# Performance work log

Hardware: AMD Instinct MI355X
Metric: run time of the kernel (lower is better)

The kernel has to match this reference:

```python
import jax, jax.numpy as jnp
import numpy as np

VOCAB = 1024
HIDDEN = 512
EMBED = 256
EPS = 1e-12  # F.normalize default eps


def setup_inputs() -> dict:
    key = jax.random.key(0)
    ks = jax.random.split(key, 7)
    B, T = 64, 16384
    tokens = jax.random.randint(ks[0], (B, T), 0, VOCAB, dtype=jnp.int64)
    # Linear params (torch nn.Linear: y = x @ W.T + b); store as [in, out] for einsum
    def lin(k, fan_in, fan_out):
        bound = 1.0 / np.sqrt(fan_in)
        kw, kb = jax.random.split(k)
        W = jax.random.uniform(kw, (fan_in, fan_out), minval=-bound, maxval=bound, dtype=jnp.float32)
        b = jax.random.uniform(kb, (fan_out,), minval=-bound, maxval=bound, dtype=jnp.float32)
        return W, b
    W1, b1 = lin(ks[1], VOCAB, HIDDEN)
    W2, b2 = lin(ks[2], HIDDEN, HIDDEN)
    W3, b3 = lin(ks[3], HIDDEN, EMBED)
    return {"tokens": tokens, "W1": W1, "b1": b1, "W2": W2, "b2": b2, "W3": W3, "b3": b3}


def reference(tokens, W1, b1, W2, b2, W3, b3):
    B, T = tokens.shape
    idx = jnp.mod(tokens, VOCAB)  # tokens % 1024
    # one_hot(...).mean(dim=1) == per-row token histogram / T; computed via scatter-add
    counts = jnp.zeros((B, VOCAB), jnp.float32).at[
        jnp.arange(B)[:, None], idx
    ].add(1.0)
    pooled = counts / jnp.asarray(T, jnp.float32)  # [B, 1024]
    h = jax.nn.relu(pooled @ W1 + b1)
    h = jax.nn.relu(h @ W2 + b2)
    emb = h @ W3 + b3  # [B, 256]
    norm = jnp.linalg.norm(emb, axis=-1, keepdims=True)
    return emb / jnp.maximum(norm, EPS)
```

## Files before the change

### kernel.cpp

```cpp
#include <hip/hip_runtime.h>
#include <hip/hip_bf16.h>


#define VOCAB 1024
#define HIDDEN 512
#define EMBED 256
#define TOK_T 16384
#define BATCH 64
#define HSEG 4

#define AGENT __HIP_MEMORY_SCOPE_AGENT

struct alignas(128) Flag { unsigned v; };

__device__ __forceinline__ void st_u32(unsigned* p, unsigned v) {
    __hip_atomic_store(p, v, __ATOMIC_RELAXED, AGENT);
}
__device__ __forceinline__ void st_f32(float* p, float v) {
    __hip_atomic_store(p, v, __ATOMIC_RELAXED, AGENT);
}

__device__ __forceinline__ void signal(Flag* flag) {
    asm volatile("s_waitcnt vmcnt(0)" ::: "memory");
    __syncthreads();
    if (threadIdx.x == 0) __hip_atomic_fetch_add(&flag->v, 1u, __ATOMIC_RELAXED, AGENT);
}
__device__ __forceinline__ void wait_flag(const Flag* flag, unsigned target) {
    if (threadIdx.x == 0) {
        while (__hip_atomic_load(&flag->v, __ATOMIC_RELAXED, AGENT) != target)
            __builtin_amdgcn_s_sleep(1);
    }
    __syncthreads();
}

#define XSIDX(k) ((k) + ((k) >> 6))

struct SMemDense {
    float4 xs4[VOCAB + VOCAB / 64];
    float part[16][4][32];
};
union SMem {
    unsigned cnt[VOCAB];
    SMemDense d;
};

template <int K, int OUT, bool RELU, bool SSQ>
__device__ __forceinline__ void dense_phase(SMem& sm, int rg, int jw,
                                            const float* __restrict__ in,
                                            const float* __restrict__ W,
                                            const float* __restrict__ bias,
                                            float* __restrict__ outp,
                                            float* __restrict__ ssqp) {
    constexpr int KG = 16;
    constexpr int KC = K / KG;
    constexpr int JW = OUT / 32;
    const int b0 = rg * 4;
    const int tid = threadIdx.x;

    for (int k = tid; k < K; k += 256) {
        float4 v;
        v.x = in[(size_t)(b0 + 0) * K + k];
        v.y = in[(size_t)(b0 + 1) * K + k];
        v.z = in[(size_t)(b0 + 2) * K + k];
        v.w = in[(size_t)(b0 + 3) * K + k];
        sm.d.xs4[XSIDX(k)] = v;
    }
    __syncthreads();

    const int jt = tid & 15;
    const int kg = tid >> 4;
    const float* __restrict__ w = W + (size_t)(kg * KC) * OUT + jw * 32 + jt * 2;

    float2 acc0 = {0.f, 0.f}, acc1 = {0.f, 0.f}, acc2 = {0.f, 0.f}, acc3 = {0.f, 0.f};
#pragma unroll 8
    for (int ks = 0; ks < KC; ++ks) {
        const int k = kg * KC + ks;
        const float4 xv = sm.d.xs4[XSIDX(k)];
        const float2 wv = *(const float2*)(w + (size_t)ks * OUT);
        acc0.x = fmaf(xv.x, wv.x, acc0.x); acc0.y = fmaf(xv.x, wv.y, acc0.y);
        acc1.x = fmaf(xv.y, wv.x, acc1.x); acc1.y = fmaf(xv.y, wv.y, acc1.y);
        acc2.x = fmaf(xv.z, wv.x, acc2.x); acc2.y = fmaf(xv.z, wv.y, acc2.y);
        acc3.x = fmaf(xv.w, wv.x, acc3.x); acc3.y = fmaf(xv.w, wv.y, acc3.y);
    }

    *(float2*)&sm.d.part[kg][0][jt * 2] = acc0;
    *(float2*)&sm.d.part[kg][1][jt * 2] = acc1;
    *(float2*)&sm.d.part[kg][2][jt * 2] = acc2;
    *(float2*)&sm.d.part[kg][3][jt * 2] = acc3;
    __syncthreads();

    if (tid < 128) {
        const int r = tid >> 5;
        const int jl = tid & 31;
        float s = bias[jw * 32 + jl];
#pragma unroll
        for (int g = 0; g < KG; ++g) s += sm.d.part[g][r][jl];
        if (RELU) s = fmaxf(s, 0.0f);
        st_f32(&outp[(size_t)(b0 + r) * OUT + jw * 32 + jl], s);
        if constexpr (SSQ) {
            float s2 = s * s;
#pragma unroll
            for (int off = 16; off > 0; off >>= 1) s2 += __shfl_down(s2, off, 32);
            if (jl == 0) st_f32(&ssqp[(size_t)(b0 + r) * JW + jw], s2);
        }
    }
}

__global__ __launch_bounds__(256) void fused_kernel(const int* __restrict__ tokens,
                                                    const float* __restrict__ W1,
                                                    const float* __restrict__ b1,
                                                    const float* __restrict__ W2,
                                                    const float* __restrict__ b2,
                                                    const float* __restrict__ W3,
                                                    const float* __restrict__ b3,
                                                    float* __restrict__ out,
                                                    unsigned* __restrict__ counts,
                                                    float* __restrict__ h1,
                                                    float* __restrict__ h2,
                                                    float* __restrict__ emb,
                                                    float* __restrict__ ssqp,
                                                    Flag* __restrict__ flagH,
                                                    Flag* __restrict__ flag1,
                                                    Flag* __restrict__ flag2,
                                                    Flag* __restrict__ flag3) {
    __shared__ SMem sm;
    const int blk = blockIdx.x;
    const int tid = threadIdx.x;

    {
        const int b = blk >> 2;
        const int seg = blk & 3;
#pragma unroll
        for (int i = 0; i < VOCAB / 256; ++i) sm.cnt[tid + 256 * i] = 0u;
        __syncthreads();

        const int4* __restrict__ t4 =
            reinterpret_cast<const int4*>(tokens + (size_t)b * TOK_T + seg * (TOK_T / HSEG));
#pragma unroll
        for (int i = 0; i < TOK_T / HSEG / 4 / 256; ++i) {
            int4 v = t4[i * 256 + tid];
            atomicAdd(&sm.cnt[v.x & (VOCAB - 1)], 1u);
            atomicAdd(&sm.cnt[v.y & (VOCAB - 1)], 1u);
            atomicAdd(&sm.cnt[v.z & (VOCAB - 1)], 1u);
            atomicAdd(&sm.cnt[v.w & (VOCAB - 1)], 1u);
        }
        __syncthreads();

        unsigned* __restrict__ row = counts + ((size_t)b * HSEG + seg) * VOCAB;
#pragma unroll
        for (int i = 0; i < 4; ++i) st_u32(&row[tid * 4 + i], sm.cnt[tid * 4 + i]);
        signal(&flagH[b]);
    }

    {
        const int rg = blk >> 4;
        const int jw = blk & 15;
        const int b0 = rg * 4;
        if (tid == 0) {
#pragma unroll
            for (int r = 0; r < 4; ++r)
                while (__hip_atomic_load(&flagH[b0 + r].v, __ATOMIC_RELAXED, AGENT) != HSEG)
                    __builtin_amdgcn_s_sleep(1);
        }
        __syncthreads();

        {
            const float invT = 1.0f / (float)TOK_T;
#pragma unroll
            for (int ko = 0; ko < 4; ++ko) {
                const int k = tid + 256 * ko;
                float4 v;
#pragma unroll
                for (int r = 0; r < 4; ++r) {
                    const unsigned* __restrict__ cr = counts + (size_t)(b0 + r) * HSEG * VOCAB;
                    unsigned s = cr[k] + cr[k + VOCAB] + cr[k + 2 * VOCAB] + cr[k + 3 * VOCAB];
                    (&v.x)[r] = (float)s * invT;
                }
                sm.d.xs4[XSIDX(k)] = v;
            }
        }
        __syncthreads();

        constexpr int K = VOCAB, OUT = HIDDEN, KG = 16, KC = K / KG;
        const int jt = tid & 15;
        const int kg = tid >> 4;
        const float* __restrict__ w = W1 + (size_t)(kg * KC) * OUT + jw * 32 + jt * 2;
        float2 acc0 = {0.f, 0.f}, acc1 = {0.f, 0.f}, acc2 = {0.f, 0.f}, acc3 = {0.f, 0.f};
#pragma unroll 8
        for (int ks = 0; ks < KC; ++ks) {
            const int k = kg * KC + ks;
            const float4 xv = sm.d.xs4[XSIDX(k)];
            const float2 wv = *(const float2*)(w + (size_t)ks * OUT);
            acc0.x = fmaf(xv.x, wv.x, acc0.x); acc0.y = fmaf(xv.x, wv.y, acc0.y);
            acc1.x = fmaf(xv.y, wv.x, acc1.x); acc1.y = fmaf(xv.y, wv.y, acc1.y);
            acc2.x = fmaf(xv.z, wv.x, acc2.x); acc2.y = fmaf(xv.z, wv.y, acc2.y);
            acc3.x = fmaf(xv.w, wv.x, acc3.x); acc3.y = fmaf(xv.w, wv.y, acc3.y);
        }
        *(float2*)&sm.d.part[kg][0][jt * 2] = acc0;
        *(float2*)&sm.d.part[kg][1][jt * 2] = acc1;
        *(float2*)&sm.d.part[kg][2][jt * 2] = acc2;
        *(float2*)&sm.d.part[kg][3][jt * 2] = acc3;
        __syncthreads();
        if (tid < 128) {
            const int r = tid >> 5;
            const int jl = tid & 31;
            float s = b1[jw * 32 + jl];
#pragma unroll
            for (int g = 0; g < KG; ++g) s += sm.d.part[g][r][jl];
            st_f32(&h1[(size_t)(b0 + r) * OUT + jw * 32 + jl], fmaxf(s, 0.0f));
        }
        signal(&flag1[rg]);
    }

    {
        const int rg = blk >> 4;
        const int jw = blk & 15;
        wait_flag(&flag1[rg], 16);
        dense_phase<HIDDEN, HIDDEN, true, false>(sm, rg, jw, h1, W2, b2, h2, nullptr);
        signal(&flag2[rg]);
    }

    if (blk < (BATCH / 4) * (EMBED / 32)) {
        const int rg = blk >> 3;
        const int jw = blk & 7;
        wait_flag(&flag2[rg], 16);
        dense_phase<HIDDEN, EMBED, false, true>(sm, rg, jw, h2, W3, b3, emb, ssqp);
        signal(&flag3[rg]);
    }

    if (blk < BATCH) {
        const int b = blk;
        wait_flag(&flag3[b >> 2], 8);
        float total = 0.0f;
#pragma unroll
        for (int i = 0; i < EMBED / 32; ++i) total += ssqp[(size_t)b * (EMBED / 32) + i];
        const float v = emb[(size_t)b * EMBED + tid];
        out[(size_t)b * EMBED + tid] = v / fmaxf(sqrtf(total), 1e-12f);
    }
}

extern "C" void kernel_launch(void* const* d_in, const int* in_sizes, int n_in,
                              void* d_out, int out_size, void* d_ws, size_t ws_size,
                              hipStream_t stream) {
    const int*   tokens = (const int*)d_in[0];
    const float* W1     = (const float*)d_in[1];
    const float* b1     = (const float*)d_in[2];
    const float* W2     = (const float*)d_in[3];
    const float* b2     = (const float*)d_in[4];
    const float* W3     = (const float*)d_in[5];
    const float* b3     = (const float*)d_in[6];
    float*       out    = (float*)d_out;

    uint8_t* base = (uint8_t*)d_ws;
    unsigned* counts = (unsigned*)(base);
    float*    h1     = (float*)(base + 0x100000);
    float*    h2     = (float*)(base + 0x120000);
    float*    emb    = (float*)(base + 0x140000);
    float*    ssqp   = (float*)(base + 0x150000);
    Flag*     flagH  = (Flag*)(base + 0x150800);
    Flag*     flag1  = flagH + BATCH;
    Flag*     flag2  = flag1 + 16;
    Flag*     flag3  = flag2 + 16;

    hipMemsetAsync((void*)flagH, 0, 112 * sizeof(Flag), stream);

    fused_kernel<<<256, 256, 0, stream>>>(tokens, W1, b1, W2, b2, W3, b3, out,
                                          counts, h1, h2, emb, ssqp,
                                          flagH, flag1, flag2, flag3);
}
```

Before: 28.40 us.

## Double block count to 512 with 2-row groups and fused final normalization

Doubles the grid from 256 to 512 blocks: histograms split each row into 8 segments, and the dense layers handle 2 batch rows per block instead of 4. This spreads weight streaming and token counting across more CUs. The separate normalization phase is folded into the last finishing block of each layer-3 row group, detected with a fetch-add ticket, which removes one flag wait stage. Smaller row groups mean each W column tile is re-read from memory by twice as many blocks, and the grid-wide spin waits now assume all 512 blocks are resident at once.

```diff
diff --git a/kernel.cpp b/kernel.cpp
--- a/kernel.cpp
+++ b/kernel.cpp
@@ -7,7 +7,7 @@
 #define EMBED 256
 #define TOK_T 16384
 #define BATCH 64
-#define HSEG 4
+#define HSEG 8
 
 #define AGENT __HIP_MEMORY_SCOPE_AGENT
 
@@ -25,19 +25,16 @@
     __syncthreads();
     if (threadIdx.x == 0) __hip_atomic_fetch_add(&flag->v, 1u, __ATOMIC_RELAXED, AGENT);
 }
-__device__ __forceinline__ void wait_flag(const Flag* flag, unsigned target) {
-    if (threadIdx.x == 0) {
-        while (__hip_atomic_load(&flag->v, __ATOMIC_RELAXED, AGENT) != target)
-            __builtin_amdgcn_s_sleep(1);
-    }
-    __syncthreads();
-}
-
-#define XSIDX(k) ((k) + ((k) >> 6))
+__device__ __forceinline__ void spin(const Flag* flag, unsigned target) {
+    while (__hip_atomic_load(&flag->v, __ATOMIC_RELAXED, AGENT) != target)
+        __builtin_amdgcn_s_sleep(1);
+}
+
+#define XSIDX(k) ((k) + ((k) >> 5))
 
 struct SMemDense {
-    float4 xs4[VOCAB + VOCAB / 64];
-    float part[16][4][32];
+    float2 xs2[VOCAB + VOCAB / 32];
+    float part[16][2][32];
 };
 union SMem {
     unsigned cnt[VOCAB];
@@ -45,51 +42,33 @@
 };
 
 template <int K, int OUT, bool RELU, bool SSQ>
-__device__ __forceinline__ void dense_phase(SMem& sm, int rg, int jw,
-                                            const float* __restrict__ in,
-                                            const float* __restrict__ W,
-                                            const float* __restrict__ bias,
-                                            float* __restrict__ outp,
-                                            float* __restrict__ ssqp) {
+__device__ __forceinline__ void dense_core(SMem& sm, int rg, int jw,
+                                           const float* __restrict__ W,
+                                           const float* __restrict__ bias,
+                                           float* __restrict__ outp,
+                                           float* __restrict__ ssqp) {
     constexpr int KG = 16;
     constexpr int KC = K / KG;
-    constexpr int JW = OUT / 32;
-    const int b0 = rg * 4;
+    const int b0 = rg * 2;
     const int tid = threadIdx.x;
-
-    for (int k = tid; k < K; k += 256) {
-        float4 v;
-        v.x = in[(size_t)(b0 + 0) * K + k];
-        v.y = in[(size_t)(b0 + 1) * K + k];
-        v.z = in[(size_t)(b0 + 2) * K + k];
-        v.w = in[(size_t)(b0 + 3) * K + k];
-        sm.d.xs4[XSIDX(k)] = v;
-    }
-    __syncthreads();
-
     const int jt = tid & 15;
     const int kg = tid >> 4;
     const float* __restrict__ w = W + (size_t)(kg * KC) * OUT + jw * 32 + jt * 2;
 
-    float2 acc0 = {0.f, 0.f}, acc1 = {0.f, 0.f}, acc2 = {0.f, 0.f}, acc3 = {0.f, 0.f};
+    float2 a0 = {0.f, 0.f}, a1 = {0.f, 0.f};
 #pragma unroll 8
     for (int ks = 0; ks < KC; ++ks) {
         const int k = kg * KC + ks;
-        const float4 xv = sm.d.xs4[XSIDX(k)];
+        const float2 x = sm.d.xs2[XSIDX(k)];
         const float2 wv = *(const float2*)(w + (size_t)ks * OUT);
-        acc0.x = fmaf(xv.x, wv.x, acc0.x); acc0.y = fmaf(xv.x, wv.y, acc0.y);
-        acc1.x = fmaf(xv.y, wv.x, acc1.x); acc1.y = fmaf(xv.y, wv.y, acc1.y);
-        acc2.x = fmaf(xv.z, wv.x, acc2.x); acc2.y = fmaf(xv.z, wv.y, acc2.y);
-        acc3.x = fmaf(xv.w, wv.x, acc3.x); acc3.y = fmaf(xv.w, wv.y, acc3.y);
-    }
-
-    *(float2*)&sm.d.part[kg][0][jt * 2] = acc0;
-    *(float2*)&sm.d.part[kg][1][jt * 2] = acc1;
-    *(float2*)&sm.d.part[kg][2][jt * 2] = acc2;
-    *(float2*)&sm.d.part[kg][3][jt * 2] = acc3;
+        a0.x = fmaf(x.x, wv.x, a0.x); a0.y = fmaf(x.x, wv.y, a0.y);
+        a1.x = fmaf(x.y, wv.x, a1.x); a1.y = fmaf(x.y, wv.y, a1.y);
+    }
+    *(float2*)&sm.d.part[kg][0][jt * 2] = a0;
+    *(float2*)&sm.d.part[kg][1][jt * 2] = a1;
     __syncthreads();
 
-    if (tid < 128) {
+    if (tid < 64) {
         const int r = tid >> 5;
         const int jl = tid & 31;
         float s = bias[jw * 32 + jl];
@@ -101,7 +80,7 @@
             float s2 = s * s;
 #pragma unroll
             for (int off = 16; off > 0; off >>= 1) s2 += __shfl_down(s2, off, 32);
-            if (jl == 0) st_f32(&ssqp[(size_t)(b0 + r) * JW + jw], s2);
+            if (jl == 0) st_f32(&ssqp[(size_t)(b0 + r) * 8 + jw], s2);
         }
     }
 }
@@ -124,12 +103,13 @@
                                                     Flag* __restrict__ flag2,
                                                     Flag* __restrict__ flag3) {
     __shared__ SMem sm;
+    __shared__ unsigned lastf;
     const int blk = blockIdx.x;
     const int tid = threadIdx.x;
 
     {
-        const int b = blk >> 2;
-        const int seg = blk & 3;
+        const int b = blk >> 3;
+        const int seg = blk & 7;
 #pragma unroll
         for (int i = 0; i < VOCAB / 256; ++i) sm.cnt[tid + 256 * i] = 0u;
         __syncthreads();
@@ -138,7 +118,7 @@
             reinterpret_cast<const int4*>(tokens + (size_t)b * TOK_T + seg * (TOK_T / HSEG));
 #pragma unroll
         for (int i = 0; i < TOK_T / HSEG / 4 / 256; ++i) {
-            int4 v = t4[i * 256 + tid];
+            int4 v = t4[tid + 256 * i];
             atomicAdd(&sm.cnt[v.x & (VOCAB - 1)], 1u);
             atomicAdd(&sm.cnt[v.y & (VOCAB - 1)], 1u);
             atomicAdd(&sm.cnt[v.z & (VOCAB - 1)], 1u);
@@ -148,19 +128,18 @@
 
         unsigned* __restrict__ row = counts + ((size_t)b * HSEG + seg) * VOCAB;
 #pragma unroll
-        for (int i = 0; i < 4; ++i) st_u32(&row[tid * 4 + i], sm.cnt[tid * 4 + i]);
+        for (int i = 0; i < VOCAB / 256; ++i)
+            st_u32(&row[tid + 256 * i], sm.cnt[tid + 256 * i]);
         signal(&flagH[b]);
     }
 
     {
         const int rg = blk >> 4;
         const int jw = blk & 15;
-        const int b0 = rg * 4;
+        const int b0 = rg * 2;
         if (tid == 0) {
-#pragma unroll
-            for (int r = 0; r < 4; ++r)
-                while (__hip_atomic_load(&flagH[b0 + r].v, __ATOMIC_RELAXED, AGENT) != HSEG)
-                    __builtin_amdgcn_s_sleep(1);
+            spin(&flagH[b0], HSEG);
+            spin(&flagH[b0 + 1], HSEG);
         }
         __syncthreads();
 
@@ -169,73 +148,80 @@
 #pragma unroll
             for (int ko = 0; ko < 4; ++ko) {
                 const int k = tid + 256 * ko;
-                float4 v;
-#pragma unroll
-                for (int r = 0; r < 4; ++r) {
-                    const unsigned* __restrict__ cr = counts + (size_t)(b0 + r) * HSEG * VOCAB;
-                    unsigned s = cr[k] + cr[k + VOCAB] + cr[k + 2 * VOCAB] + cr[k + 3 * VOCAB];
-                    (&v.x)[r] = (float)s * invT;
+                unsigned s0 = 0, s1 = 0;
+#pragma unroll
+                for (int sg = 0; sg < HSEG; ++sg) {
+                    s0 += counts[((size_t)(b0 + 0) * HSEG + sg) * VOCAB + k];
+                    s1 += counts[((size_t)(b0 + 1) * HSEG + sg) * VOCAB + k];
                 }
-                sm.d.xs4[XSIDX(k)] = v;
+                float2 v = {(float)s0 * invT, (float)s1 * invT};
+                sm.d.xs2[XSIDX(k)] = v;
             }
         }
         __syncthreads();
 
-        constexpr int K = VOCAB, OUT = HIDDEN, KG = 16, KC = K / KG;
-        const int jt = tid & 15;
-        const int kg = tid >> 4;
-        const float* __restrict__ w = W1 + (size_t)(kg * KC) * OUT + jw * 32 + jt * 2;
-        float2 acc0 = {0.f, 0.f}, acc1 = {0.f, 0.f}, acc2 = {0.f, 0.f}, acc3 = {0.f, 0.f};
-#pragma unroll 8
-        for (int ks = 0; ks < KC; ++ks) {
-            const int k = kg * KC + ks;
-            const float4 xv = sm.d.xs4[XSIDX(k)];
-            const float2 wv = *(const float2*)(w + (size_t)ks * OUT);
-            acc0.x = fmaf(xv.x, wv.x, acc0.x); acc0.y = fmaf(xv.x, wv.y, acc0.y);
-            acc1.x = fmaf(xv.y, wv.x, acc1.x); acc1.y = fmaf(xv.y, wv.y, acc1.y);
-            acc2.x = fmaf(xv.z, wv.x, acc2.x); acc2.y = fmaf(xv.z, wv.y, acc2.y);
-            acc3.x = fmaf(xv.w, wv.x, acc3.x); acc3.y = fmaf(xv.w, wv.y, acc3.y);
-        }
-        *(float2*)&sm.d.part[kg][0][jt * 2] = acc0;
-        *(float2*)&sm.d.part[kg][1][jt * 2] = acc1;
-        *(float2*)&sm.d.part[kg][2][jt * 2] = acc2;
-        *(float2*)&sm.d.part[kg][3][jt * 2] = acc3;
-        __syncthreads();
-        if (tid < 128) {
-            const int r = tid >> 5;
-            const int jl = tid & 31;
-            float s = b1[jw * 32 + jl];
-#pragma unroll
-            for (int g = 0; g < KG; ++g) s += sm.d.part[g][r][jl];
-            st_f32(&h1[(size_t)(b0 + r) * OUT + jw * 32 + jl], fmaxf(s, 0.0f));
-        }
+        dense_core<VOCAB, HIDDEN, true, false>(sm, rg, jw, W1, b1, h1, nullptr);
         signal(&flag1[rg]);
     }
 
     {
         const int rg = blk >> 4;
         const int jw = blk & 15;
-        wait_flag(&flag1[rg], 16);
-        dense_phase<HIDDEN, HIDDEN, true, false>(sm, rg, jw, h1, W2, b2, h2, nullptr);
+        const int b0 = rg * 2;
+        if (tid == 0) spin(&flag1[rg], 16);
+        __syncthreads();
+
+#pragma unroll
+        for (int ko = 0; ko < 2; ++ko) {
+            const int k = tid + 256 * ko;
+            float2 v;
+            v.x = h1[(size_t)(b0 + 0) * HIDDEN + k];
+            v.y = h1[(size_t)(b0 + 1) * HIDDEN + k];
+            sm.d.xs2[XSIDX(k)] = v;
+        }
+        __syncthreads();
+
+        dense_core<HIDDEN, HIDDEN, true, false>(sm, rg, jw, W2, b2, h2, nullptr);
         signal(&flag2[rg]);
     }
 
-    if (blk < (BATCH / 4) * (EMBED / 32)) {
+    if (blk < 256) {
         const int rg = blk >> 3;
         const int jw = blk & 7;
-        wait_flag(&flag2[rg], 16);
-        dense_phase<HIDDEN, EMBED, false, true>(sm, rg, jw, h2, W3, b3, emb, ssqp);
-        signal(&flag3[rg]);
-    }
-
-    if (blk < BATCH) {
-        const int b = blk;
-        wait_flag(&flag3[b >> 2], 8);
-        float total = 0.0f;
-#pragma unroll
-        for (int i = 0; i < EMBED / 32; ++i) total += ssqp[(size_t)b * (EMBED / 32) + i];
-        const float v = emb[(size_t)b * EMBED + tid];
-        out[(size_t)b * EMBED + tid] = v / fmaxf(sqrtf(total), 1e-12f);
+        const int b0 = rg * 2;
+        if (tid == 0) spin(&flag2[rg], 16);
+        __syncthreads();
+
+#pragma unroll
+        for (int ko = 0; ko < 2; ++ko) {
+            const int k = tid + 256 * ko;
+            float2 v;
+            v.x = h2[(size_t)(b0 + 0) * HIDDEN + k];
+            v.y = h2[(size_t)(b0 + 1) * HIDDEN + k];
+            sm.d.xs2[XSIDX(k)] = v;
+        }
+        __syncthreads();
+
+        dense_core<HIDDEN, EMBED, false, true>(sm, rg, jw, W3, b3, emb, ssqp);
+
+        asm volatile("s_waitcnt vmcnt(0)" ::: "memory");
+        __syncthreads();
+        if (tid == 0)
+            lastf = (__hip_atomic_fetch_add(&flag3[rg].v, 1u, __ATOMIC_RELAXED, AGENT) == 7u);
+        __syncthreads();
+
+        if (lastf) {
+            const int r = tid >> 7;
+            const int j2 = (tid & 127) * 2;
+            float total = 0.0f;
+#pragma unroll
+            for (int i = 0; i < 8; ++i) total += ssqp[(size_t)(b0 + r) * 8 + i];
+            const float scale = 1.0f / fmaxf(sqrtf(total), 1e-12f);
+            const float e0 = emb[(size_t)(b0 + r) * EMBED + j2];
+            const float e1 = emb[(size_t)(b0 + r) * EMBED + j2 + 1];
+            out[(size_t)(b0 + r) * EMBED + j2] = e0 * scale;
+            out[(size_t)(b0 + r) * EMBED + j2 + 1] = e1 * scale;
+        }
     }
 }
 
@@ -253,18 +239,18 @@
 
     uint8_t* base = (uint8_t*)d_ws;
     unsigned* counts = (unsigned*)(base);
-    float*    h1     = (float*)(base + 0x100000);
-    float*    h2     = (float*)(base + 0x120000);
-    float*    emb    = (float*)(base + 0x140000);
-    float*    ssqp   = (float*)(base + 0x150000);
-    Flag*     flagH  = (Flag*)(base + 0x150800);
+    float*    h1     = (float*)(base + 0x200000);
+    float*    h2     = (float*)(base + 0x220000);
+    float*    emb    = (float*)(base + 0x240000);
+    float*    ssqp   = (float*)(base + 0x250000);
+    Flag*     flagH  = (Flag*)(base + 0x250800);
     Flag*     flag1  = flagH + BATCH;
-    Flag*     flag2  = flag1 + 16;
-    Flag*     flag3  = flag2 + 16;
-
-    hipMemsetAsync((void*)flagH, 0, 112 * sizeof(Flag), stream);
-
-    fused_kernel<<<256, 256, 0, stream>>>(tokens, W1, b1, W2, b2, W3, b3, out,
+    Flag*     flag2  = flag1 + 32;
+    Flag*     flag3  = flag2 + 32;
+
+    hipMemsetAsync((void*)flagH, 0, 160 * sizeof(Flag), stream);
+
+    fused_kernel<<<512, 256, 0, stream>>>(tokens, W1, b1, W2, b2, W3, b3, out,
                                           counts, h1, h2, emb, ssqp,
                                           flagH, flag1, flag2, flag3);
 }
```

After: 34.01 us. 1.2x slower.

## Split fused kernel at dense1 and fold normalization into last dense3 block

Applied to the files above, without the earlier changes.

Splits the single persistent kernel into two launches: histogram plus first dense layer, then dense2, dense3 and normalization. The flag1 grid barrier is replaced by the kernel boundary. The separate normalization phase is dropped: the last block to finish each row group's dense3 normalizes those rows using float4 stores. This trades an extra launch for fewer spin-wait barriers and one less stage of cross-block waiting.

```diff
diff --git a/kernel.cpp b/kernel.cpp
--- a/kernel.cpp
+++ b/kernel.cpp
@@ -25,12 +25,9 @@
     __syncthreads();
     if (threadIdx.x == 0) __hip_atomic_fetch_add(&flag->v, 1u, __ATOMIC_RELAXED, AGENT);
 }
-__device__ __forceinline__ void wait_flag(const Flag* flag, unsigned target) {
-    if (threadIdx.x == 0) {
-        while (__hip_atomic_load(&flag->v, __ATOMIC_RELAXED, AGENT) != target)
-            __builtin_amdgcn_s_sleep(1);
-    }
-    __syncthreads();
+__device__ __forceinline__ void spin(const Flag* flag, unsigned target) {
+    while (__hip_atomic_load(&flag->v, __ATOMIC_RELAXED, AGENT) != target)
+        __builtin_amdgcn_s_sleep(1);
 }
 
 #define XSIDX(k) ((k) + ((k) >> 6))
@@ -44,7 +41,7 @@
     SMemDense d;
 };
 
-template <int K, int OUT, bool RELU, bool SSQ>
+template <int K, int OUT, bool RELU, bool SSQ, bool PLAIN_OUT>
 __device__ __forceinline__ void dense_phase(SMem& sm, int rg, int jw,
                                             const float* __restrict__ in,
                                             const float* __restrict__ W,
@@ -96,7 +93,8 @@
 #pragma unroll
         for (int g = 0; g < KG; ++g) s += sm.d.part[g][r][jl];
         if (RELU) s = fmaxf(s, 0.0f);
-        st_f32(&outp[(size_t)(b0 + r) * OUT + jw * 32 + jl], s);
+        if (PLAIN_OUT) outp[(size_t)(b0 + r) * OUT + jw * 32 + jl] = s;
+        else           st_f32(&outp[(size_t)(b0 + r) * OUT + jw * 32 + jl], s);
         if constexpr (SSQ) {
             float s2 = s * s;
 #pragma unroll
@@ -106,23 +104,12 @@
     }
 }
 
-__global__ __launch_bounds__(256) void fused_kernel(const int* __restrict__ tokens,
-                                                    const float* __restrict__ W1,
-                                                    const float* __restrict__ b1,
-                                                    const float* __restrict__ W2,
-                                                    const float* __restrict__ b2,
-                                                    const float* __restrict__ W3,
-                                                    const float* __restrict__ b3,
-                                                    float* __restrict__ out,
-                                                    unsigned* __restrict__ counts,
-                                                    float* __restrict__ h1,
-                                                    float* __restrict__ h2,
-                                                    float* __restrict__ emb,
-                                                    float* __restrict__ ssqp,
-                                                    Flag* __restrict__ flagH,
-                                                    Flag* __restrict__ flag1,
-                                                    Flag* __restrict__ flag2,
-                                                    Flag* __restrict__ flag3) {
+__global__ __launch_bounds__(256) void k1_hist_dense1(const int* __restrict__ tokens,
+                                                      const float* __restrict__ W1,
+                                                      const float* __restrict__ b1,
+                                                      unsigned* __restrict__ counts,
+                                                      float* __restrict__ h1,
+                                                      Flag* __restrict__ flagH) {
     __shared__ SMem sm;
     const int blk = blockIdx.x;
     const int tid = threadIdx.x;
@@ -158,9 +145,7 @@
         const int b0 = rg * 4;
         if (tid == 0) {
 #pragma unroll
-            for (int r = 0; r < 4; ++r)
-                while (__hip_atomic_load(&flagH[b0 + r].v, __ATOMIC_RELAXED, AGENT) != HSEG)
-                    __builtin_amdgcn_s_sleep(1);
+            for (int r = 0; r < 4; ++r) spin(&flagH[b0 + r], HSEG);
         }
         __syncthreads();
 
@@ -207,35 +192,61 @@
             float s = b1[jw * 32 + jl];
 #pragma unroll
             for (int g = 0; g < KG; ++g) s += sm.d.part[g][r][jl];
-            st_f32(&h1[(size_t)(b0 + r) * OUT + jw * 32 + jl], fmaxf(s, 0.0f));
-        }
-        signal(&flag1[rg]);
-    }
+            h1[(size_t)(b0 + r) * OUT + jw * 32 + jl] = fmaxf(s, 0.0f);
+        }
+    }
+}
+
+__global__ __launch_bounds__(256) void k2_dense23_norm(const float* __restrict__ h1,
+                                                       const float* __restrict__ W2,
+                                                       const float* __restrict__ b2,
+                                                       const float* __restrict__ W3,
+                                                       const float* __restrict__ b3,
+                                                       float* __restrict__ out,
+                                                       float* __restrict__ h2,
+                                                       float* __restrict__ emb,
+                                                       float* __restrict__ ssqp,
+                                                       Flag* __restrict__ flag2,
+                                                       Flag* __restrict__ flag3) {
+    __shared__ SMem sm;
+    __shared__ unsigned lastf;
+    const int blk = blockIdx.x;
+    const int tid = threadIdx.x;
 
     {
         const int rg = blk >> 4;
         const int jw = blk & 15;
-        wait_flag(&flag1[rg], 16);
-        dense_phase<HIDDEN, HIDDEN, true, false>(sm, rg, jw, h1, W2, b2, h2, nullptr);
+        dense_phase<HIDDEN, HIDDEN, true, false, false>(sm, rg, jw, h1, W2, b2, h2, nullptr);
         signal(&flag2[rg]);
     }
 
     if (blk < (BATCH / 4) * (EMBED / 32)) {
         const int rg = blk >> 3;
         const int jw = blk & 7;
-        wait_flag(&flag2[rg], 16);
-        dense_phase<HIDDEN, EMBED, false, true>(sm, rg, jw, h2, W3, b3, emb, ssqp);
-        signal(&flag3[rg]);
-    }
-
-    if (blk < BATCH) {
-        const int b = blk;
-        wait_flag(&flag3[b >> 2], 8);
-        float total = 0.0f;
-#pragma unroll
-        for (int i = 0; i < EMBED / 32; ++i) total += ssqp[(size_t)b * (EMBED / 32) + i];
-        const float v = emb[(size_t)b * EMBED + tid];
-        out[(size_t)b * EMBED + tid] = v / fmaxf(sqrtf(total), 1e-12f);
+        const int b0 = rg * 4;
+        if (tid == 0) spin(&flag2[rg], 16);
+        __syncthreads();
+
+        dense_phase<HIDDEN, EMBED, false, true, false>(sm, rg, jw, h2, W3, b3, emb, ssqp);
+
+        asm volatile("s_waitcnt vmcnt(0)" ::: "memory");
+        __syncthreads();
+        if (tid == 0)
+            lastf = (__hip_atomic_fetch_add(&flag3[rg].v, 1u, __ATOMIC_RELAXED, AGENT) == 7u);
+        __syncthreads();
+
+        if (lastf) {
+            const int r = tid >> 6;
+            const int j4 = (tid & 63) * 4;
+            const int row = b0 + r;
+            float total = 0.0f;
+#pragma unroll
+            for (int i = 0; i < 8; ++i) total += ssqp[(size_t)row * 8 + i];
+            const float scale = 1.0f / fmaxf(sqrtf(total), 1e-12f);
+            const float4 e = *(const float4*)&emb[(size_t)row * EMBED + j4];
+            float4 o = {e.x * scale, e.y * scale, e.z * scale, e.w * scale};
+            *(float4*)&out[(size_t)row * EMBED + j4] = o;
+        }
     }
 }
 
@@ -258,13 +269,12 @@
     float*    emb    = (float*)(base + 0x140000);
     float*    ssqp   = (float*)(base + 0x150000);
     Flag*     flagH  = (Flag*)(base + 0x150800);
-    Flag*     flag1  = flagH + BATCH;
-    Flag*     flag2  = flag1 + 16;
+    Flag*     flag2  = flagH + BATCH;
     Flag*     flag3  = flag2 + 16;
 
-    hipMemsetAsync((void*)flagH, 0, 112 * sizeof(Flag), stream);
-
-    fused_kernel<<<256, 256, 0, stream>>>(tokens, W1, b1, W2, b2, W3, b3, out,
-                                          counts, h1, h2, emb, ssqp,
-                                          flagH, flag1, flag2, flag3);
-}
+    hipMemsetAsync((void*)flagH, 0, 96 * sizeof(Flag), stream);
+
+    k1_hist_dense1<<<256, 256, 0, stream>>>(tokens, W1, b1, counts, h1, flagH);
+    k2_dense23_norm<<<256, 256, 0, stream>>>(h1, W2, b2, W3, b3, out,
+                                             h2, emb, ssqp, flag2, flag3);
+}
```

After: 27.81 us. -2.1%, faster.
